# Performance work log

Measured on AMD Instinct MI355X. Metric: run time of the kernel, lower is better.

## Reference

```python
import jax, jax.numpy as jnp
from jax import lax
import numpy as np

B, S, D, H = 256, 2048, 16, 128
HH = H // 2  # head hidden = 64


def _p(key, shape, scale=0.05):
    return scale * jax.random.normal(key, shape, dtype=jnp.float32)


def setup_inputs() -> dict:
    key = jax.random.key(0)
    ks = jax.random.split(key, 12)
    return {
        "x": jax.random.normal(ks[0], (B, S, D), dtype=jnp.float32),
        # LSTM layer 0 (PyTorch gate order: i, f, g, o along the 4H axis)
        "W_ih0": _p(ks[1], (4 * H, D)),
        "W_hh0": _p(ks[2], (4 * H, H)),
        "b_ih0": jnp.zeros((4 * H,), jnp.float32),
        "b_hh0": jnp.zeros((4 * H,), jnp.float32),
        # LSTM layer 1
        "W_ih1": _p(ks[3], (4 * H, H)),
        "W_hh1": _p(ks[4], (4 * H, H)),
        "b_ih1": jnp.zeros((4 * H,), jnp.float32),
        "b_hh1": jnp.zeros((4 * H,), jnp.float32),
        # return head: Linear(H, H//2) -> LeakyReLU -> Linear(H//2, 1)
        "Wr1": _p(ks[5], (HH, H)), "br1": jnp.zeros((HH,), jnp.float32),
        "Wr2": _p(ks[6], (1, HH)), "br2": jnp.zeros((1,), jnp.float32),
        # vol head: Linear -> LeakyReLU -> Linear -> Softplus
        "Wv1": _p(ks[7], (HH, H)), "bv1": jnp.zeros((HH,), jnp.float32),
        "Wv2": _p(ks[8], (1, HH)), "bv2": jnp.zeros((1,), jnp.float32),
    }


def _lstm_layer(x, W_ih, W_hh, b_ih, b_hh):
    # x: (B, S, Din) -> hs: (B, S, H); PyTorch gate order i, f, g, o
    b, s, _ = x.shape
    h_dim = W_hh.shape[1]
    xg = jnp.einsum('bsd,gd->bsg', x, W_ih) + (b_ih + b_hh)  # (B, S, 4H)

    def step(carry, xg_t):
        h, c = carry
        g = xg_t + h @ W_hh.T
        i, f, gc, o = jnp.split(g, 4, axis=-1)
        i = jax.nn.sigmoid(i)
        f = jax.nn.sigmoid(f)
        gc = jnp.tanh(gc)
        o = jax.nn.sigmoid(o)
        c = f * c + i * gc
        h = o * jnp.tanh(c)
        return (h, c), h

    h0 = jnp.zeros((b, h_dim), x.dtype)
    (hN, cN), hs = lax.scan(step, (h0, jnp.zeros_like(h0)), jnp.swapaxes(xg, 0, 1))
    return jnp.swapaxes(hs, 0, 1), hN, cN


def reference(x, W_ih0, W_hh0, b_ih0, b_hh0, W_ih1, W_hh1, b_ih1, b_hh1,
              Wr1, br1, Wr2, br2, Wv1, bv1, Wv2, bv2):
    h1, hN0, cN0 = _lstm_layer(x, W_ih0, W_hh0, b_ih0, b_hh0)
    # inter-layer dropout is inactive at inference (eval mode)
    h2, hN1, cN1 = _lstm_layer(h1, W_ih1, W_hh1, b_ih1, b_hh1)
    # return head
    r = jax.nn.leaky_relu(jnp.einsum('bsh,kh->bsk', h2, Wr1) + br1)
    returns = jnp.einsum('bsk,ok->bso', r, Wr2) + br2
    # volatility head
    v = jax.nn.leaky_relu(jnp.einsum('bsh,kh->bsk', h2, Wv1) + bv1)
    volatility = jax.nn.softplus(jnp.einsum('bsk,ok->bso', v, Wv2) + bv2)
    hidden_h = jnp.stack([hN0, hN1], axis=0)  # (num_layers, B, H)
    hidden_c = jnp.stack([cN0, cN1], axis=0)
    return returns, volatility, hidden_h, hidden_c
```

## Files before the change

kernel.cpp:

```cpp
#include <hip/hip_runtime.h>
#include <hip/hip_bf16.h>

#define B_ 256
#define S_ 2048
#define D_ 16
#define H_ 128

typedef unsigned int u32;
typedef unsigned short u16;
typedef _Float16 h2t __attribute__((ext_vector_type(2)));

#define RET0 ((size_t)0)
#define VOL0 ((size_t)524288)
#define HH0  ((size_t)1048576)
#define HC0  ((size_t)1114112)

__device__ __forceinline__ float fdot2(u32 a, u32 b, float c) {
    return __builtin_amdgcn_fdot2(__builtin_bit_cast(h2t, a),
                                  __builtin_bit_cast(h2t, b), c, false);
}
__device__ __forceinline__ u32 packh2(float a, float b) {
    h2t h; h[0] = (_Float16)a; h[1] = (_Float16)b;
    return __builtin_bit_cast(u32, h);
}
__device__ __forceinline__ float sigm(float x) {
    return __builtin_amdgcn_rcpf(1.f + __builtin_amdgcn_exp2f(-1.44269504f * x));
}
__device__ __forceinline__ float tanh_(float x) {
    return 2.f * __builtin_amdgcn_rcpf(1.f + __builtin_amdgcn_exp2f(-2.88539008f * x)) - 1.f;
}
__device__ __forceinline__ float softplus_(float x) {
    if (x > 20.f) return x;
    const float e = __builtin_amdgcn_exp2f(1.44269504f * x);
    return 0.69314718f * __builtin_amdgcn_logf(1.f + e);
}
__device__ __forceinline__ float dxor1(float a) {
    return __builtin_bit_cast(float, __builtin_amdgcn_update_dpp(
        0, __builtin_bit_cast(int, a), 0xB1, 0xF, 0xF, true));
}
__device__ __forceinline__ float dxor2(float a) {
    return __builtin_bit_cast(float, __builtin_amdgcn_update_dpp(
        0, __builtin_bit_cast(int, a), 0x4E, 0xF, 0xF, true));
}
__device__ __forceinline__ float dhalf(float a) {
    return __builtin_bit_cast(float, __builtin_amdgcn_update_dpp(
        0, __builtin_bit_cast(int, a), 0x141, 0xF, 0xF, true));
}
__device__ __forceinline__ float dror8(float a) {
    return __builtin_bit_cast(float, __builtin_amdgcn_update_dpp(
        0, __builtin_bit_cast(int, a), 0x128, 0xF, 0xF, true));
}
#define REDUCE8D(a) { a += dxor1(a); a += dxor2(a); a += dhalf(a); }

__global__
__attribute__((amdgpu_waves_per_eu(4, 4)))
__launch_bounds__(1024) void k_l0(
    const float* __restrict__ x, const float* __restrict__ Wih,
    const float* __restrict__ Whh, const float* __restrict__ bih,
    const float* __restrict__ bhh, u32* __restrict__ h1out,
    float* __restrict__ out)
{
    __shared__ u32 xp2[2][4096];
    __shared__ u32 hb[2][64];
    __shared__ u32 och[4096];

    const int tid = threadIdx.x, b = blockIdx.x;
    const int m = tid >> 3, ksl = tid & 7;

    u32 wx[4], wh[32];
    float bias[4];
#pragma unroll
    for (int g = 0; g < 4; ++g) {
        const int row = g * H_ + m;
        const float2 f2 = *(const float2*)(Wih + row * D_ + ksl * 2);
        wx[g] = packh2(f2.x, f2.y);
        const float4* whr = (const float4*)(Whh + row * H_ + ksl * 16);
#pragma unroll
        for (int j = 0; j < 4; ++j) {
            const float4 f = whr[j];
            wh[g * 8 + 2 * j]     = packh2(f.x, f.y);
            wh[g * 8 + 2 * j + 1] = packh2(f.z, f.w);
        }
        bias[g] = bih[row] + bhh[row];
    }

    const float* xb = x + (size_t)b * S_ * D_;
    for (int i = tid; i < 2048; i += 1024) {
        const float4 v = *(const float4*)(xb + i * 4);
        xp2[0][2 * i] = packh2(v.x, v.y);
        xp2[0][2 * i + 1] = packh2(v.z, v.w);
    }
    if (tid < 128) ((u32*)hb)[tid] = 0u;
    float c = 0.f;
    __syncthreads();

    for (int t = 0; t < S_; ++t) {
        if ((t & 511) == 0 && t < S_ - 512) {
            const int nw = (t >> 9) + 1;
            u32* dst = xp2[nw & 1];
            const float* src = xb + (size_t)nw * 8192;
            for (int i = tid; i < 2048; i += 1024) {
                const float4 v = *(const float4*)(src + i * 4);
                dst[2 * i] = packh2(v.x, v.y);
                dst[2 * i + 1] = packh2(v.z, v.w);
            }
        }
        const u32 xv = xp2[(t >> 9) & 1][(t & 511) * 8 + ksl];
        const u32* hsel = &hb[(t + 1) & 1][ksl * 8];
        const uint4 h0 = *(const uint4*)(hsel);
        const uint4 h1v = *(const uint4*)(hsel + 4);

        float a0 = fdot2(xv, wx[0], 0.f), a1 = fdot2(xv, wx[1], 0.f);
        float a2 = fdot2(xv, wx[2], 0.f), a3 = fdot2(xv, wx[3], 0.f);
#define L0G(comp, j)                                                           \
        a0 = fdot2(comp, wh[j], a0);        a1 = fdot2(comp, wh[8 + (j)], a1); \
        a2 = fdot2(comp, wh[16 + (j)], a2); a3 = fdot2(comp, wh[24 + (j)], a3);
        L0G(h0.x, 0) L0G(h0.y, 1) L0G(h0.z, 2) L0G(h0.w, 3)
        L0G(h1v.x, 4) L0G(h1v.y, 5) L0G(h1v.z, 6) L0G(h1v.w, 7)
#undef L0G
        REDUCE8D(a0) REDUCE8D(a1) REDUCE8D(a2) REDUCE8D(a3)
        const float ig = sigm(a0 + bias[0]);
        const float fg = sigm(a1 + bias[1]);
        const float gc = tanh_(a2 + bias[2]);
        const float og = sigm(a3 + bias[3]);
        c = fg * c + ig * gc;
        const float hv = og * tanh_(c);
        const u32 pp = packh2(hv, dror8(hv));
        if ((tid & 15) == 0) {
            hb[t & 1][m >> 1] = pp;
            och[(t & 63) * 64 + (m >> 1)] = pp;
        }
        if (t == S_ - 1 && (tid & 7) == 0) {
            out[HH0 + (size_t)b * H_ + m] = hv;
            out[HC0 + (size_t)b * H_ + m] = c;
        }
        __syncthreads();
        if ((t & 63) == 63) {
            u32* dst = h1out + ((size_t)b * S_ + (t - 63)) * 64;
            *(uint4*)(dst + tid * 4) = *(const uint4*)(&och[tid * 4]);
            __syncthreads();
        }
    }
}

__global__
__attribute__((amdgpu_waves_per_eu(4, 4)))
__launch_bounds__(1024) void k_l1full(
    u32* __restrict__ hws,
    const float* __restrict__ Wih, const float* __restrict__ Whh,
    const float* __restrict__ bih, const float* __restrict__ bhh,
    float* __restrict__ out)
{
    __shared__ u32 h1w[128 * 80];
    __shared__ u32 hp[2][80];
    __shared__ u32 och[4096];

    const int tid = threadIdx.x, b = blockIdx.x;
    const int m = tid >> 3, ksl = tid & 7;

    u32 w[64];
    float bias[4];
    const float* Wsel = (ksl < 4) ? Wih : Whh;
    const int colb = (ksl & 3) * 32;
#pragma unroll
    for (int g = 0; g < 4; ++g) {
        const int row = g * H_ + m;
        const float4* wr_ = (const float4*)(Wsel + row * H_ + colb);
#pragma unroll
        for (int j = 0; j < 8; ++j) {
            const float4 f = wr_[j];
            w[g * 16 + 2 * j]     = packh2(f.x, f.y);
            w[g * 16 + 2 * j + 1] = packh2(f.z, f.w);
        }
        bias[g] = bih[row] + bhh[row];
    }

    if (tid < 160) ((u32*)hp)[tid] = 0u;
    float c = 0.f;
    __syncthreads();

    u32* hbase = hws + (size_t)b * S_ * 64;
    for (int u = 0; u < S_; ++u) {
        if ((u & 127) == 0) {
            for (int i = tid; i < 2048; i += 1024) {
                const uint4 v = *(const uint4*)(hbase + (size_t)u * 64 + i * 4);
                const int st = i >> 4, p4 = i & 15;
                *(uint4*)(&h1w[st * 80 + (p4 >> 2) * 20 + (p4 & 3) * 4]) = v;
            }
            __syncthreads();
        }
        const u32* sel = (ksl < 4) ? &h1w[(u & 127) * 80 + ksl * 20]
                                   : &hp[(u + 1) & 1][(ksl - 4) * 20];
        float a0 = 0.f, a1 = 0.f, a2 = 0.f, a3 = 0.f;
#pragma unroll
        for (int p = 0; p < 4; ++p) {
            const uint4 v = *(const uint4*)(sel + p * 4);
            a0 = fdot2(v.x, w[4 * p], a0);      a0 = fdot2(v.y, w[4 * p + 1], a0);
            a0 = fdot2(v.z, w[4 * p + 2], a0);  a0 = fdot2(v.w, w[4 * p + 3], a0);
            a1 = fdot2(v.x, w[16 + 4 * p], a1); a1 = fdot2(v.y, w[17 + 4 * p], a1);
            a1 = fdot2(v.z, w[18 + 4 * p], a1); a1 = fdot2(v.w, w[19 + 4 * p], a1);
            a2 = fdot2(v.x, w[32 + 4 * p], a2); a2 = fdot2(v.y, w[33 + 4 * p], a2);
            a2 = fdot2(v.z, w[34 + 4 * p], a2); a2 = fdot2(v.w, w[35 + 4 * p], a2);
            a3 = fdot2(v.x, w[48 + 4 * p], a3); a3 = fdot2(v.y, w[49 + 4 * p], a3);
            a3 = fdot2(v.z, w[50 + 4 * p], a3); a3 = fdot2(v.w, w[51 + 4 * p], a3);
        }
        REDUCE8D(a0) REDUCE8D(a1) REDUCE8D(a2) REDUCE8D(a3)
        const float ig = sigm(a0 + bias[0]);
        const float fg = sigm(a1 + bias[1]);
        const float gc = tanh_(a2 + bias[2]);
        const float og = sigm(a3 + bias[3]);
        c = fg * c + ig * gc;
        const float hv = og * tanh_(c);
        const u32 pp = packh2(hv, dror8(hv));
        if ((tid & 15) == 0) {
            const int m2 = m >> 1;
            hp[u & 1][(m2 >> 4) * 20 + (m2 & 15)] = pp;
            och[(u & 63) * 64 + m2] = pp;
        }
        if (u == S_ - 1 && (tid & 7) == 0) {
            out[HH0 + 32768 + (size_t)b * H_ + m] = hv;
            out[HC0 + 32768 + (size_t)b * H_ + m] = c;
        }
        __syncthreads();
        if ((u & 63) == 63) {
            u32* dst = hbase + (size_t)(u - 63) * 64;
            *(uint4*)(dst + tid * 4) = *(const uint4*)(&och[tid * 4]);
            __syncthreads();
        }
    }
}

__global__
__attribute__((amdgpu_waves_per_eu(4, 4)))
__launch_bounds__(256) void k_heads(
    const u32* __restrict__ h2p,
    const float* __restrict__ Wr1, const float* __restrict__ br1,
    const float* __restrict__ Wr2, const float* __restrict__ br2,
    const float* __restrict__ Wv1, const float* __restrict__ bv1,
    const float* __restrict__ Wv2, const float* __restrict__ bv2,
    float* __restrict__ out)
{
    __shared__ u32 wr[64 * 64], wv[64 * 64];
    __shared__ float w2r[64], w2v[64], b1r[64], b1v[64];

    const int tid = threadIdx.x;
    for (int i = tid; i < 4096; i += 256) {
        wr[i] = packh2(Wr1[2 * i], Wr1[2 * i + 1]);
        wv[i] = packh2(Wv1[2 * i], Wv1[2 * i + 1]);
    }
    if (tid < 64) {
        w2r[tid] = Wr2[tid]; w2v[tid] = Wv2[tid];
        b1r[tid] = br1[tid]; b1v[tid] = bv1[tid];
    }
    __syncthreads();

    const size_t bs = (size_t)blockIdx.x * 256 + tid;
    u32 hq[64];
    const u32* src = h2p + bs * 64;
#pragma unroll
    for (int j4 = 0; j4 < 16; ++j4) {
        const uint4 v = *(const uint4*)(src + j4 * 4);
        hq[j4 * 4] = v.x; hq[j4 * 4 + 1] = v.y; hq[j4 * 4 + 2] = v.z; hq[j4 * 4 + 3] = v.w;
    }
    float ret = br2[0], vol = bv2[0];
    for (int k = 0; k < 64; ++k) {
        float r = b1r[k], v = b1v[k];
#pragma unroll
        for (int j = 0; j < 64; ++j) r = fdot2(hq[j], wr[k * 64 + j], r);
#pragma unroll
        for (int j = 0; j < 64; ++j) v = fdot2(hq[j], wv[k * 64 + j], v);
        r = r > 0.f ? r : 0.01f * r;
        v = v > 0.f ? v : 0.01f * v;
        ret += r * w2r[k];
        vol += v * w2v[k];
    }
    out[RET0 + bs] = ret;
    out[VOL0 + bs] = softplus_(vol);
}

extern "C" void kernel_launch(void* const* d_in, const int* in_sizes, int n_in,
                              void* d_out, int out_size, void* d_ws, size_t ws_size,
                              hipStream_t stream) {
    (void)in_sizes; (void)n_in; (void)out_size; (void)ws_size;
    const float* x    = (const float*)d_in[0];
    const float* Wih0 = (const float*)d_in[1];
    const float* Whh0 = (const float*)d_in[2];
    const float* bih0 = (const float*)d_in[3];
    const float* bhh0 = (const float*)d_in[4];
    const float* Wih1 = (const float*)d_in[5];
    const float* Whh1 = (const float*)d_in[6];
    const float* bih1 = (const float*)d_in[7];
    const float* bhh1 = (const float*)d_in[8];
    const float* Wr1  = (const float*)d_in[9];
    const float* br1  = (const float*)d_in[10];
    const float* Wr2  = (const float*)d_in[11];
    const float* br2  = (const float*)d_in[12];
    const float* Wv1  = (const float*)d_in[13];
    const float* bv1  = (const float*)d_in[14];
    const float* Wv2  = (const float*)d_in[15];
    const float* bv2  = (const float*)d_in[16];
    u32* hws  = (u32*)d_ws;
    float* out = (float*)d_out;

    k_l0<<<B_, 1024, 0, stream>>>(x, Wih0, Whh0, bih0, bhh0, hws, out);
    k_l1full<<<B_, 1024, 0, stream>>>(hws, Wih1, Whh1, bih1, bhh1, out);
    k_heads<<<2048, 256, 0, stream>>>(hws, Wr1, br1, Wr2, br2,
                                      Wv1, bv1, Wv2, bv2, out);
}
```

Measured before the change: 3.962 ms.

## Replace DPP cross-lane gate reduction with LDS partial sums in LSTM kernels

Both LSTM recurrence kernels now put the 8 k-slices of each hidden unit in separate waves (ksl = tid>>7) instead of adjacent lanes. Each thread writes its four partial gate sums to shared memory, and after a barrier the first 128 threads add them and apply the gate nonlinearities. This replaces the DPP butterfly reduction and stops 8x redundant activation math, but adds a second __syncthreads per timestep and leaves the nonlinear phase on only two waves. Shared-memory staging buffers are halved, with x reloaded every 256 steps, h1 every 64 steps and output flushed every 32 steps.

```diff
diff --git a/kernel.cpp b/kernel.cpp
--- a/kernel.cpp
+++ b/kernel.cpp
@@ -34,23 +34,10 @@
     const float e = __builtin_amdgcn_exp2f(1.44269504f * x);
     return 0.69314718f * __builtin_amdgcn_logf(1.f + e);
 }
-__device__ __forceinline__ float dxor1(float a) {
+__device__ __forceinline__ float dnb1(float a) {
     return __builtin_bit_cast(float, __builtin_amdgcn_update_dpp(
         0, __builtin_bit_cast(int, a), 0xB1, 0xF, 0xF, true));
 }
-__device__ __forceinline__ float dxor2(float a) {
-    return __builtin_bit_cast(float, __builtin_amdgcn_update_dpp(
-        0, __builtin_bit_cast(int, a), 0x4E, 0xF, 0xF, true));
-}
-__device__ __forceinline__ float dhalf(float a) {
-    return __builtin_bit_cast(float, __builtin_amdgcn_update_dpp(
-        0, __builtin_bit_cast(int, a), 0x141, 0xF, 0xF, true));
-}
-__device__ __forceinline__ float dror8(float a) {
-    return __builtin_bit_cast(float, __builtin_amdgcn_update_dpp(
-        0, __builtin_bit_cast(int, a), 0x128, 0xF, 0xF, true));
-}
-#define REDUCE8D(a) { a += dxor1(a); a += dxor2(a); a += dhalf(a); }
 
 __global__
 __attribute__((amdgpu_waves_per_eu(4, 4)))
@@ -60,15 +47,15 @@
     const float* __restrict__ bhh, u32* __restrict__ h1out,
     float* __restrict__ out)
 {
-    __shared__ u32 xp2[2][4096];
+    __shared__ u32 xp2[2][2048];
+    __shared__ float gates[8][128][4];
     __shared__ u32 hb[2][64];
-    __shared__ u32 och[4096];
+    __shared__ u32 och[2048];
 
     const int tid = threadIdx.x, b = blockIdx.x;
-    const int m = tid >> 3, ksl = tid & 7;
+    const int ksl = tid >> 7, m = tid & 127;
 
     u32 wx[4], wh[32];
-    float bias[4];
 #pragma unroll
     for (int g = 0; g < 4; ++g) {
         const int row = g * H_ + m;
@@ -81,35 +68,33 @@
             wh[g * 8 + 2 * j]     = packh2(f.x, f.y);
             wh[g * 8 + 2 * j + 1] = packh2(f.z, f.w);
         }
-        bias[g] = bih[row] + bhh[row];
+    }
+    float bias[4], c = 0.f;
+    if (tid < 128) {
+#pragma unroll
+        for (int g = 0; g < 4; ++g) bias[g] = bih[g * H_ + tid] + bhh[g * H_ + tid];
     }
 
     const float* xb = x + (size_t)b * S_ * D_;
-    for (int i = tid; i < 2048; i += 1024) {
-        const float4 v = *(const float4*)(xb + i * 4);
-        xp2[0][2 * i] = packh2(v.x, v.y);
-        xp2[0][2 * i + 1] = packh2(v.z, v.w);
+    {
+        const float4 v = *(const float4*)(xb + tid * 4);
+        xp2[0][2 * tid] = packh2(v.x, v.y);
+        xp2[0][2 * tid + 1] = packh2(v.z, v.w);
     }
     if (tid < 128) ((u32*)hb)[tid] = 0u;
-    float c = 0.f;
     __syncthreads();
 
     for (int t = 0; t < S_; ++t) {
-        if ((t & 511) == 0 && t < S_ - 512) {
-            const int nw = (t >> 9) + 1;
-            u32* dst = xp2[nw & 1];
-            const float* src = xb + (size_t)nw * 8192;
-            for (int i = tid; i < 2048; i += 1024) {
-                const float4 v = *(const float4*)(src + i * 4);
-                dst[2 * i] = packh2(v.x, v.y);
-                dst[2 * i + 1] = packh2(v.z, v.w);
-            }
-        }
-        const u32 xv = xp2[(t >> 9) & 1][(t & 511) * 8 + ksl];
-        const u32* hsel = &hb[(t + 1) & 1][ksl * 8];
-        const uint4 h0 = *(const uint4*)(hsel);
-        const uint4 h1v = *(const uint4*)(hsel + 4);
-
+        if ((t & 255) == 0 && t < S_ - 256) {
+            const int nw = (t >> 8) + 1;
+            const float4 v = *(const float4*)(xb + (size_t)nw * 4096 + tid * 4);
+            xp2[nw & 1][2 * tid] = packh2(v.x, v.y);
+            xp2[nw & 1][2 * tid + 1] = packh2(v.z, v.w);
+        }
+        const u32 xv = xp2[(t >> 8) & 1][(t & 255) * 8 + ksl];
+        const u32* hs = &hb[(t + 1) & 1][ksl * 8];
+        const uint4 h0 = *(const uint4*)(hs);
+        const uint4 h1v = *(const uint4*)(hs + 4);
         float a0 = fdot2(xv, wx[0], 0.f), a1 = fdot2(xv, wx[1], 0.f);
         float a2 = fdot2(xv, wx[2], 0.f), a3 = fdot2(xv, wx[3], 0.f);
 #define L0G(comp, j)                                                           \
@@ -118,26 +103,38 @@
         L0G(h0.x, 0) L0G(h0.y, 1) L0G(h0.z, 2) L0G(h0.w, 3)
         L0G(h1v.x, 4) L0G(h1v.y, 5) L0G(h1v.z, 6) L0G(h1v.w, 7)
 #undef L0G
-        REDUCE8D(a0) REDUCE8D(a1) REDUCE8D(a2) REDUCE8D(a3)
-        const float ig = sigm(a0 + bias[0]);
-        const float fg = sigm(a1 + bias[1]);
-        const float gc = tanh_(a2 + bias[2]);
-        const float og = sigm(a3 + bias[3]);
-        c = fg * c + ig * gc;
-        const float hv = og * tanh_(c);
-        const u32 pp = packh2(hv, dror8(hv));
-        if ((tid & 15) == 0) {
-            hb[t & 1][m >> 1] = pp;
-            och[(t & 63) * 64 + (m >> 1)] = pp;
-        }
-        if (t == S_ - 1 && (tid & 7) == 0) {
-            out[HH0 + (size_t)b * H_ + m] = hv;
-            out[HC0 + (size_t)b * H_ + m] = c;
-        }
+        float4 part; part.x = a0; part.y = a1; part.z = a2; part.w = a3;
+        *(float4*)&gates[ksl][m][0] = part;
         __syncthreads();
-        if ((t & 63) == 63) {
-            u32* dst = h1out + ((size_t)b * S_ + (t - 63)) * 64;
-            *(uint4*)(dst + tid * 4) = *(const uint4*)(&och[tid * 4]);
+        if (tid < 128) {
+            float4 s = *(const float4*)&gates[0][tid][0];
+#pragma unroll
+            for (int k = 1; k < 8; ++k) {
+                const float4 p = *(const float4*)&gates[k][tid][0];
+                s.x += p.x; s.y += p.y; s.z += p.z; s.w += p.w;
+            }
+            const float ig = sigm(s.x + bias[0]);
+            const float fg = sigm(s.y + bias[1]);
+            const float gc = tanh_(s.z + bias[2]);
+            const float og = sigm(s.w + bias[3]);
+            c = fg * c + ig * gc;
+            const float hv = og * tanh_(c);
+            const u32 pp = packh2(hv, dnb1(hv));
+            if (!(tid & 1)) {
+                hb[t & 1][tid >> 1] = pp;
+                och[(t & 31) * 64 + (tid >> 1)] = pp;
+            }
+            if (t == S_ - 1) {
+                out[HH0 + (size_t)b * H_ + tid] = hv;
+                out[HC0 + (size_t)b * H_ + tid] = c;
+            }
+        }
+        __syncthreads();
+        if ((t & 31) == 31) {
+            if (tid < 512) {
+                u32* dst = h1out + ((size_t)b * S_ + (t - 31)) * 64;
+                *(uint4*)(dst + tid * 4) = *(const uint4*)(&och[tid * 4]);
+            }
             __syncthreads();
         }
     }
@@ -145,21 +142,21 @@
 
 __global__
 __attribute__((amdgpu_waves_per_eu(4, 4)))
-__launch_bounds__(1024) void k_l1full(
+__launch_bounds__(1024) void k_l1(
     u32* __restrict__ hws,
     const float* __restrict__ Wih, const float* __restrict__ Whh,
     const float* __restrict__ bih, const float* __restrict__ bhh,
     float* __restrict__ out)
 {
-    __shared__ u32 h1w[128 * 80];
+    __shared__ u32 h1w[64 * 80];
+    __shared__ float gates[8][128][4];
     __shared__ u32 hp[2][80];
-    __shared__ u32 och[4096];
+    __shared__ u32 och[2048];
 
     const int tid = threadIdx.x, b = blockIdx.x;
-    const int m = tid >> 3, ksl = tid & 7;
+    const int ksl = tid >> 7, m = tid & 127;
 
     u32 w[64];
-    float bias[4];
     const float* Wsel = (ksl < 4) ? Wih : Whh;
     const int colb = (ksl & 3) * 32;
 #pragma unroll
@@ -172,24 +169,24 @@
             w[g * 16 + 2 * j]     = packh2(f.x, f.y);
             w[g * 16 + 2 * j + 1] = packh2(f.z, f.w);
         }
-        bias[g] = bih[row] + bhh[row];
-    }
-
+    }
+    float bias[4], c = 0.f;
+    if (tid < 128) {
+#pragma unroll
+        for (int g = 0; g < 4; ++g) bias[g] = bih[g * H_ + tid] + bhh[g * H_ + tid];
+    }
     if (tid < 160) ((u32*)hp)[tid] = 0u;
-    float c = 0.f;
     __syncthreads();
 
     u32* hbase = hws + (size_t)b * S_ * 64;
     for (int u = 0; u < S_; ++u) {
-        if ((u & 127) == 0) {
-            for (int i = tid; i < 2048; i += 1024) {
-                const uint4 v = *(const uint4*)(hbase + (size_t)u * 64 + i * 4);
-                const int st = i >> 4, p4 = i & 15;
-                *(uint4*)(&h1w[st * 80 + (p4 >> 2) * 20 + (p4 & 3) * 4]) = v;
-            }
+        if ((u & 63) == 0) {
+            const uint4 v = *(const uint4*)(hbase + (size_t)u * 64 + tid * 4);
+            const int st = tid >> 4, p4 = tid & 15;
+            *(uint4*)(&h1w[st * 80 + (p4 >> 2) * 20 + (p4 & 3) * 4]) = v;
             __syncthreads();
         }
-        const u32* sel = (ksl < 4) ? &h1w[(u & 127) * 80 + ksl * 20]
+        const u32* sel = (ksl < 4) ? &h1w[(u & 63) * 80 + ksl * 20]
                                    : &hp[(u + 1) & 1][(ksl - 4) * 20];
         float a0 = 0.f, a1 = 0.f, a2 = 0.f, a3 = 0.f;
 #pragma unroll
@@ -204,35 +201,45 @@
             a3 = fdot2(v.x, w[48 + 4 * p], a3); a3 = fdot2(v.y, w[49 + 4 * p], a3);
             a3 = fdot2(v.z, w[50 + 4 * p], a3); a3 = fdot2(v.w, w[51 + 4 * p], a3);
         }
-        REDUCE8D(a0) REDUCE8D(a1) REDUCE8D(a2) REDUCE8D(a3)
-        const float ig = sigm(a0 + bias[0]);
-        const float fg = sigm(a1 + bias[1]);
-        const float gc = tanh_(a2 + bias[2]);
-        const float og = sigm(a3 + bias[3]);
-        c = fg * c + ig * gc;
-        const float hv = og * tanh_(c);
-        const u32 pp = packh2(hv, dror8(hv));
-        if ((tid & 15) == 0) {
-            const int m2 = m >> 1;
-            hp[u & 1][(m2 >> 4) * 20 + (m2 & 15)] = pp;
-            och[(u & 63) * 64 + m2] = pp;
-        }
-        if (u == S_ - 1 && (tid & 7) == 0) {
-            out[HH0 + 32768 + (size_t)b * H_ + m] = hv;
-            out[HC0 + 32768 + (size_t)b * H_ + m] = c;
-        }
+        float4 part; part.x = a0; part.y = a1; part.z = a2; part.w = a3;
+        *(float4*)&gates[ksl][m][0] = part;
         __syncthreads();
-        if ((u & 63) == 63) {
-            u32* dst = hbase + (size_t)(u - 63) * 64;
-            *(uint4*)(dst + tid * 4) = *(const uint4*)(&och[tid * 4]);
+        if (tid < 128) {
+            float4 s = *(const float4*)&gates[0][tid][0];
+#pragma unroll
+            for (int k = 1; k < 8; ++k) {
+                const float4 p = *(const float4*)&gates[k][tid][0];
+                s.x += p.x; s.y += p.y; s.z += p.z; s.w += p.w;
+            }
+            const float ig = sigm(s.x + bias[0]);
+            const float fg = sigm(s.y + bias[1]);
+            const float gc = tanh_(s.z + bias[2]);
+            const float og = sigm(s.w + bias[3]);
+            c = fg * c + ig * gc;
+            const float hv = og * tanh_(c);
+            const u32 pp = packh2(hv, dnb1(hv));
+            if (!(tid & 1)) {
+                const int p2 = tid >> 1;
+                hp[u & 1][(p2 >> 4) * 20 + (p2 & 15)] = pp;
+                och[(u & 31) * 64 + p2] = pp;
+            }
+            if (u == S_ - 1) {
+                out[HH0 + 32768 + (size_t)b * H_ + tid] = hv;
+                out[HC0 + 32768 + (size_t)b * H_ + tid] = c;
+            }
+        }
+        __syncthreads();
+        if ((u & 31) == 31) {
+            if (tid < 512) {
+                u32* dst = hbase + (size_t)(u - 31) * 64;
+                *(uint4*)(dst + tid * 4) = *(const uint4*)(&och[tid * 4]);
+            }
             __syncthreads();
         }
     }
 }
 
-__global__
-__attribute__((amdgpu_waves_per_eu(4, 4)))
-__launch_bounds__(256) void k_heads(
+__global__ __launch_bounds__(256) void k_heads(
     const u32* __restrict__ h2p,
     const float* __restrict__ Wr1, const float* __restrict__ br1,
     const float* __restrict__ Wr2, const float* __restrict__ br2,
@@ -303,7 +310,7 @@
     float* out = (float*)d_out;
 
     k_l0<<<B_, 1024, 0, stream>>>(x, Wih0, Whh0, bih0, bhh0, hws, out);
-    k_l1full<<<B_, 1024, 0, stream>>>(hws, Wih1, Whh1, bih1, bhh1, out);
+    k_l1<<<B_, 1024, 0, stream>>>(hws, Wih1, Whh1, bih1, bhh1, out);
     k_heads<<<2048, 256, 0, stream>>>(hws, Wr1, br1, Wr2, br2,
                                       Wv1, bv1, Wv2, bv2, out);
 }
```

Measured after the change: 3.554 ms. 10.3% less time.
